# Optimization experiments

Measured on AMD Instinct MI355X. Metric: run time of the kernel, lower is better.

## Reference

```python
import jax, jax.numpy as jnp
import numpy as np

N_NODES = 100000
N_EDGES = 1250000
IN_CH = 64
OUT_CH = 64


def setup_inputs() -> dict:
    key = jax.random.key(0)
    k1, k2, k3 = jax.random.split(key, 3)
    x = jax.random.normal(k1, (N_NODES, IN_CH), dtype=jnp.float32)
    edge_index = jax.random.randint(k2, (2, N_EDGES), 0, N_NODES, dtype=jnp.int64)
    # torch.nn.Linear(3*IN_CH, OUT_CH): W [out, in], b [out]
    scale = 1.0 / np.sqrt(3 * IN_CH)
    W = jax.random.uniform(k3, (OUT_CH, 3 * IN_CH), dtype=jnp.float32,
                           minval=-scale, maxval=scale)
    b = jnp.zeros((OUT_CH,), dtype=jnp.float32)
    return {"x": x, "edge_index": edge_index, "W": W, "b": b}


def reference(x, edge_index, W, b):
    src, dst = edge_index[0], edge_index[1]
    msgs = x[src]  # [E, D] gather of source node features

    agg_sum = jax.ops.segment_sum(msgs, dst, num_segments=N_NODES)  # [N, D]
    count = jax.ops.segment_sum(jnp.ones((msgs.shape[0],), dtype=x.dtype),
                                dst, num_segments=N_NODES)  # [N]
    agg_mean = agg_sum / jnp.maximum(count, 1.0)[:, None]

    agg_max = jax.ops.segment_max(msgs, dst, num_segments=N_NODES)  # [N, D]
    has_edge = (count > 0)[:, None]
    agg_max = jnp.where(has_edge, agg_max, 0.0)  # empty segments -> 0 (PyG default)

    feats = jnp.concatenate([agg_sum, agg_mean, agg_max], axis=-1)  # [N, 3D]
    return jnp.einsum('nf,of->no', feats, W) + b
```

## Files before the change

kernel.cpp:

```cpp
#include <hip/hip_runtime.h>
#include <hip/hip_bf16.h>
#include <math.h>

#define D    64
#define F3   192
#define FS   128
#define NPB  256
#define LBITS 8
#define SBITS 17
#define NBLK 256
#define SCAN_CHUNK 2048
#define BUCKET_PAD 1800
#define SSRC_CAP   2000000

using bf16x8 = __attribute__((ext_vector_type(8))) short;
using f32x4  = __attribute__((ext_vector_type(4))) float;

__device__ __forceinline__ ushort f2bf(float f) {
    __hip_bfloat16 h = __float2bfloat16(f);
    return *reinterpret_cast<ushort*>(&h);
}
__device__ __forceinline__ float bf2f(ushort u) {
    unsigned v = ((unsigned)u) << 16;
    return __uint_as_float(v);
}

__global__ __launch_bounds__(256) void k_cast_hist(
    const float* __restrict__ x, ushort* __restrict__ xb, int n4,
    const float* __restrict__ W, ushort* __restrict__ Wb, int nW,
    const int* __restrict__ dstv, unsigned* __restrict__ bcntT,
    int E, int EPB, int NB, int castBlocks)
{
    int bid = blockIdx.x;
    if (bid < NBLK) {
        __shared__ unsigned h[512];
        for (int i = threadIdx.x; i < NB; i += 256) h[i] = 0;
        __syncthreads();
        int lo = bid * EPB, hi = min(E, lo + EPB);
        for (int e = lo + threadIdx.x; e < hi; e += 256)
            atomicAdd(&h[((unsigned)dstv[e]) >> LBITS], 1u);
        __syncthreads();
        for (int i = threadIdx.x; i < NB; i += 256)
            bcntT[(size_t)i * NBLK + bid] = h[i];
    } else if (bid < NBLK + castBlocks) {
        int i = (bid - NBLK) * 256 + threadIdx.x;
        if (i < n4) {
            float4 v = *reinterpret_cast<const float4*>(x + (size_t)i * 4);
            ushort4 u = { f2bf(v.x), f2bf(v.y), f2bf(v.z), f2bf(v.w) };
            *reinterpret_cast<ushort4*>(xb + (size_t)i * 4) = u;
        }
    } else {
        for (int i = threadIdx.x; i < nW; i += 256) Wb[i] = f2bf(W[i]);
    }
}

__global__ __launch_bounds__(256) void k_chunk_scan(
    const unsigned* __restrict__ cnt, unsigned* __restrict__ offs,
    unsigned* __restrict__ partials, int N)
{
    __shared__ unsigned ts[256];
    int t = threadIdx.x;
    int ebase = blockIdx.x * SCAN_CHUNK + t * 8;
    unsigned v[8];
    unsigned s = 0;
    #pragma unroll
    for (int j = 0; j < 8; ++j) {
        unsigned c = (ebase + j < N) ? cnt[ebase + j] : 0u;
        v[j] = s; s += c;
    }
    ts[t] = s;
    __syncthreads();
    #pragma unroll
    for (int off = 1; off < 256; off <<= 1) {
        unsigned add = (t >= off) ? ts[t - off] : 0u;
        __syncthreads();
        ts[t] += add;
        __syncthreads();
    }
    unsigned tb = (t > 0) ? ts[t - 1] : 0u;
    #pragma unroll
    for (int j = 0; j < 8; ++j)
        if (ebase + j < N) offs[ebase + j] = tb + v[j];
    if (t == 255) partials[blockIdx.x] = ts[255];
}

__device__ __forceinline__ void scan_partials_lds(
    const unsigned* __restrict__ partials, unsigned* psc, int n, int t)
{
    __shared__ unsigned raw[64];
    if (t < n) raw[t] = partials[t];
    __syncthreads();
    if (t == 0) {
        unsigned s = 0;
        for (int i = 0; i < n; ++i) { unsigned c = raw[i]; psc[i] = s; s += c; }
    }
    __syncthreads();
}

__global__ __launch_bounds__(256) void k_bin_scatter(
    const int* __restrict__ srcv, const int* __restrict__ dstv,
    const unsigned* __restrict__ bbaseT, const unsigned* __restrict__ partials,
    int nChunks, unsigned* __restrict__ binned, int E, int EPB, int NB)
{
    __shared__ unsigned cur[512];
    __shared__ unsigned psc[64];
    int t = threadIdx.x;
    scan_partials_lds(partials, psc, nChunks, t);
    for (int i = t; i < NB; i += 256) {
        unsigned idx = (unsigned)i * NBLK + blockIdx.x;
        cur[i] = bbaseT[idx] + psc[idx >> 11];
    }
    __syncthreads();
    int lo = blockIdx.x * EPB, hi = min(E, lo + EPB);
    for (int e = lo + t; e < hi; e += 256) {
        unsigned d = (unsigned)dstv[e];
        unsigned s = (unsigned)srcv[e];
        unsigned p = atomicAdd(&cur[d >> LBITS], 1u);
        binned[p] = ((d & (NPB - 1u)) << SBITS) | s;
    }
}

__global__ __launch_bounds__(256) void k_bucket_csr(
    const unsigned* __restrict__ binned, const unsigned* __restrict__ bbaseT,
    const unsigned* __restrict__ partials, int nChunks,
    unsigned* __restrict__ offs, unsigned* __restrict__ cnt,
    unsigned* __restrict__ ssrc, int E, int NB, int N)
{
    __shared__ unsigned c[256];
    __shared__ unsigned ts[256];
    __shared__ unsigned psc[64];
    int k = blockIdx.x;
    int t = threadIdx.x;
    scan_partials_lds(partials, psc, nChunks, t);

    unsigned i0 = (unsigned)k * NBLK;
    unsigned bstart = bbaseT[i0] + psc[i0 >> 11];
    unsigned bend;
    if (k + 1 < NB) {
        unsigned i1 = (unsigned)(k + 1) * NBLK;
        bend = bbaseT[i1] + psc[i1 >> 11];
    } else bend = (unsigned)E;
    unsigned bstartPad = ((bstart + 7u) & ~7u) + (unsigned)BUCKET_PAD * k;

    c[t] = 0;
    __syncthreads();
    for (unsigned e = bstart + t; e < bend; e += 256)
        atomicAdd(&c[binned[e] >> SBITS], 1u);
    __syncthreads();

    unsigned myc  = c[t];
    unsigned mycp = (myc + 7u) & ~7u;
    ts[t] = mycp;
    __syncthreads();
    #pragma unroll
    for (int off = 1; off < 256; off <<= 1) {
        unsigned add = (t >= off) ? ts[t - off] : 0u;
        __syncthreads();
        ts[t] += add;
        __syncthreads();
    }
    unsigned exclp = t ? ts[t - 1] : 0u;
    unsigned stPad = bstartPad + exclp;

    int gn = k * NPB + t;
    if (gn < N) { offs[gn] = stPad; cnt[gn] = myc; }

    c[t] = exclp;
    __syncthreads();
    for (unsigned e = bstart + t; e < bend; e += 256) {
        unsigned u  = binned[e];
        unsigned ld = u >> SBITS;
        unsigned r  = atomicAdd(&c[ld], 1u);
        ssrc[bstartPad + r] = u & ((1u << SBITS) - 1u);
    }
    __syncthreads();
    if (myc && mycp > myc) {
        unsigned lastId = ssrc[stPad + myc - 1];
        for (unsigned j = myc; j < mycp; ++j) ssrc[stPad + j] = lastId;
    }
}

__global__ __launch_bounds__(256) void k_gather5(
    const ushort*   __restrict__ xb,
    const unsigned* __restrict__ ssrc,
    const unsigned* __restrict__ offs,
    const unsigned* __restrict__ cnt,
    ushort*         __restrict__ feats,
    int N)
{
    const unsigned* xw = reinterpret_cast<const unsigned*>(xb);
    unsigned* fw = reinterpret_cast<unsigned*>(feats);

    int tid  = threadIdx.x;
    unsigned lane = tid & 63;
    unsigned l31  = lane & 31;
    bool     hi   = lane >= 32;
    int wv   = tid >> 6;

    int nq = (N + 3) >> 2;
    for (int q = blockIdx.x; q < nq; q += gridDim.x) {
        int n = q * 4 + wv;
        if (n >= N) continue;

        unsigned st  = offs[n];
        unsigned dg  = cnt[n];
        unsigned dgp = (dg + 7u) & ~7u;

        float se0 = 0.f, so0 = 0.f, se1 = 0.f, so1 = 0.f;
        float me0 = -INFINITY, mo0 = -INFINITY, me1 = -INFINITY, mo1 = -INFINITY;

        unsigned i = 0;
        for (; i + 16 <= dgp; i += 16) {
            uint4 ia = *reinterpret_cast<const uint4*>(ssrc + st + i);
            uint4 ib = *reinterpret_cast<const uint4*>(ssrc + st + i + 4);
            uint4 ic = *reinterpret_cast<const uint4*>(ssrc + st + i + 8);
            uint4 id = *reinterpret_cast<const uint4*>(ssrc + st + i + 12);
            unsigned p0 = hi ? ia.y : ia.x;
            unsigned p1 = hi ? ia.w : ia.z;
            unsigned p2 = hi ? ib.y : ib.x;
            unsigned p3 = hi ? ib.w : ib.z;
            unsigned p4 = hi ? ic.y : ic.x;
            unsigned p5 = hi ? ic.w : ic.z;
            unsigned p6 = hi ? id.y : id.x;
            unsigned p7 = hi ? id.w : id.z;
            unsigned w0 = xw[(p0 << 5) | l31];
            unsigned w1 = xw[(p1 << 5) | l31];
            unsigned w2 = xw[(p2 << 5) | l31];
            unsigned w3 = xw[(p3 << 5) | l31];
            unsigned w4 = xw[(p4 << 5) | l31];
            unsigned w5 = xw[(p5 << 5) | l31];
            unsigned w6 = xw[(p6 << 5) | l31];
            unsigned w7 = xw[(p7 << 5) | l31];
            #pragma unroll
            for (int j = 0; j < 8; ++j) {
                unsigned w = (j==0)?w0:(j==1)?w1:(j==2)?w2:(j==3)?w3:
                             (j==4)?w4:(j==5)?w5:(j==6)?w6:w7;
                float fe = __uint_as_float(w << 16);
                float fo = __uint_as_float(w & 0xFFFF0000u);
                if (j & 1) {
                    se1 += fe; so1 += fo;
                    me1 = fmaxf(me1, fe); mo1 = fmaxf(mo1, fo);
                } else {
                    se0 += fe; so0 += fo;
                    me0 = fmaxf(me0, fe); mo0 = fmaxf(mo0, fo);
                }
            }
        }
        if (i < dgp) {
            uint4 ia = *reinterpret_cast<const uint4*>(ssrc + st + i);
            uint4 ib = *reinterpret_cast<const uint4*>(ssrc + st + i + 4);
            unsigned p0 = hi ? ia.y : ia.x;
            unsigned p1 = hi ? ia.w : ia.z;
            unsigned p2 = hi ? ib.y : ib.x;
            unsigned p3 = hi ? ib.w : ib.z;
            unsigned w0 = xw[(p0 << 5) | l31];
            unsigned w1 = xw[(p1 << 5) | l31];
            unsigned w2 = xw[(p2 << 5) | l31];
            unsigned w3 = xw[(p3 << 5) | l31];
            #pragma unroll
            for (int j = 0; j < 4; ++j) {
                unsigned w = (j==0)?w0:(j==1)?w1:(j==2)?w2:w3;
                float fe = __uint_as_float(w << 16);
                float fo = __uint_as_float(w & 0xFFFF0000u);
                if (j & 1) {
                    se1 += fe; so1 += fo;
                    me1 = fmaxf(me1, fe); mo1 = fmaxf(mo1, fo);
                } else {
                    se0 += fe; so0 += fo;
                    me0 = fmaxf(me0, fe); mo0 = fmaxf(mo0, fo);
                }
            }
        }

        float se = se0 + se1, so = so0 + so1;
        float me = fmaxf(me0, me1), mo = fmaxf(mo0, mo1);
        se += __shfl_xor(se, 32);
        so += __shfl_xor(so, 32);
        me = fmaxf(me, __shfl_xor(me, 32));
        mo = fmaxf(mo, __shfl_xor(mo, 32));

        unsigned p = dgp - dg;
        if (p && dg) {
            unsigned lastId = ssrc[st + dg - 1];
            unsigned w = xw[(lastId << 5) | l31];
            se -= (float)p * __uint_as_float(w << 16);
            so -= (float)p * __uint_as_float(w & 0xFFFF0000u);
        }
        if (!dg) { me = 0.0f; mo = 0.0f; }

        float v0 = hi ? me : se;
        float v1 = hi ? mo : so;
        unsigned outw = ((unsigned)f2bf(v0)) | (((unsigned)f2bf(v1)) << 16);
        fw[((size_t)n << 6) | lane] = outw;
    }
}

__global__ __launch_bounds__(256) void k_mlp2(
    const ushort*   __restrict__ feats,
    const unsigned* __restrict__ cnt,
    const ushort*   __restrict__ Wb,
    const float*    __restrict__ bias,
    float*          __restrict__ out,
    int N)
{
    int tid  = threadIdx.x;
    int lane = tid & 63;
    int wv   = tid >> 6;
    int l16  = lane & 15;
    int kb   = (lane >> 4) << 3;

    int col = (wv << 4) + l16;
    const ushort* wp = Wb + (size_t)col * F3 + kb;
    bf16x8 bS0 = *reinterpret_cast<const bf16x8*>(wp);
    bf16x8 bS1 = *reinterpret_cast<const bf16x8*>(wp + 32);
    bf16x8 bM0 = *reinterpret_cast<const bf16x8*>(wp + 64);
    bf16x8 bM1 = *reinterpret_cast<const bf16x8*>(wp + 96);
    bf16x8 bX0 = *reinterpret_cast<const bf16x8*>(wp + 128);
    bf16x8 bX1 = *reinterpret_cast<const bf16x8*>(wp + 160);
    float bo = bias[col];

    int n0 = blockIdx.x << 4;

    unsigned dgr = cnt[n0 + l16];
    float inv = dgr ? 1.0f / (float)dgr : 0.0f;

    const ushort* arow = feats + (size_t)(n0 + l16) * FS + kb;
    bf16x8 aS0 = *reinterpret_cast<const bf16x8*>(arow);
    bf16x8 aS1 = *reinterpret_cast<const bf16x8*>(arow + 32);
    bf16x8 aX0 = *reinterpret_cast<const bf16x8*>(arow + 64);
    bf16x8 aX1 = *reinterpret_cast<const bf16x8*>(arow + 96);

    bf16x8 aM0, aM1;
    #pragma unroll
    for (int j = 0; j < 8; ++j) {
        aM0[j] = (short)f2bf(bf2f((ushort)aS0[j]) * inv);
        aM1[j] = (short)f2bf(bf2f((ushort)aS1[j]) * inv);
    }

    f32x4 acc = { bo, bo, bo, bo };
    acc = __builtin_amdgcn_mfma_f32_16x16x32_bf16(aS0, bS0, acc, 0, 0, 0);
    acc = __builtin_amdgcn_mfma_f32_16x16x32_bf16(aS1, bS1, acc, 0, 0, 0);
    acc = __builtin_amdgcn_mfma_f32_16x16x32_bf16(aM0, bM0, acc, 0, 0, 0);
    acc = __builtin_amdgcn_mfma_f32_16x16x32_bf16(aM1, bM1, acc, 0, 0, 0);
    acc = __builtin_amdgcn_mfma_f32_16x16x32_bf16(aX0, bX0, acc, 0, 0, 0);
    acc = __builtin_amdgcn_mfma_f32_16x16x32_bf16(aX1, bX1, acc, 0, 0, 0);

    int rbase = n0 + ((lane >> 4) << 2);
    #pragma unroll
    for (int r = 0; r < 4; ++r)
        out[(size_t)(rbase + r) * D + col] = acc[r];
}

extern "C" void kernel_launch(void* const* d_in, const int* in_sizes, int n_in,
                              void* d_out, int out_size, void* d_ws, size_t ws_size,
                              hipStream_t stream)
{
    const float* x  = (const float*)d_in[0];
    const int*   ei = (const int*)d_in[1];
    const float* W  = (const float*)d_in[2];
    const float* b  = (const float*)d_in[3];
    float* out = (float*)d_out;

    int N = in_sizes[0] / D;
    int E = in_sizes[1] / 2;
    const int* srcv = ei;
    const int* dstv = ei + E;

    int NB  = (N + NPB - 1) / NPB;
    int EPB = (E + NBLK - 1) / NBLK;
    int M   = NB * NBLK;

    unsigned* bcntT    = (unsigned*)d_ws;
    unsigned* bbaseT   = bcntT + M;
    unsigned* partials = bbaseT + M;
    unsigned* offs     = partials + 64;
    unsigned* cnt      = offs + N;
    unsigned* ssrc     = cnt + N;
    ushort*   xb       = (ushort*)(ssrc + SSRC_CAP);
    ushort*   Wb       = xb + (size_t)N * D;
    ushort*   feats    = Wb + (size_t)D * F3;
    unsigned* binned   = (unsigned*)feats;

    int nChunksM  = (M + SCAN_CHUNK - 1) / SCAN_CHUNK;
    int n4        = N * D / 4;
    int castBlocks = (n4 + 255) / 256;

    k_cast_hist<<<NBLK + castBlocks + 1, 256, 0, stream>>>(
        x, xb, n4, W, Wb, D * F3, dstv, bcntT, E, EPB, NB, castBlocks);
    k_chunk_scan<<<nChunksM, 256, 0, stream>>>(bcntT, bbaseT, partials, M);
    k_bin_scatter<<<NBLK, 256, 0, stream>>>(srcv, dstv, bbaseT, partials,
                                            nChunksM, binned, E, EPB, NB);
    k_bucket_csr<<<NB, 256, 0, stream>>>(binned, bbaseT, partials, nChunksM,
                                         offs, cnt, ssrc, E, NB, N);
    k_gather5<<<2048, 256, 0, stream>>>(xb, ssrc, offs, cnt, feats, N);
    k_mlp2<<<N / 16, 256, 0, stream>>>(feats, cnt, Wb, b, out, N);
}
```

Before: 114.4 us.

## Fuse neighbor gather aggregation with MFMA linear layer via LDS tile

Merges the gather/aggregate kernel and the MFMA projection kernel into one. Each wave aggregates sum and max for 16 nodes into a swizzled LDS tile, then runs the bf16 MFMA projection for all 64 output columns directly from that tile. This removes the global round trip of the intermediate features buffer and one kernel launch. However, all four waves in a block use the same tile index and never use their wave id to choose nodes. They therefore repeat the same gather work and write identical outputs, which multiplies the dominant irregular gather cost.

```diff
diff --git a/kernel.cpp b/kernel.cpp
--- a/kernel.cpp
+++ b/kernel.cpp
@@ -4,7 +4,6 @@
 
 #define D    64
 #define F3   192
-#define FS   128
 #define NPB  256
 #define LBITS 8
 #define SBITS 17
@@ -180,175 +179,178 @@
     }
 }
 
-__global__ __launch_bounds__(256) void k_gather5(
+__global__ __launch_bounds__(256) void k_gather_mlp(
     const ushort*   __restrict__ xb,
     const unsigned* __restrict__ ssrc,
     const unsigned* __restrict__ offs,
     const unsigned* __restrict__ cnt,
-    ushort*         __restrict__ feats,
+    const ushort*   __restrict__ Wb,
+    const float*    __restrict__ bias,
+    float*          __restrict__ out,
     int N)
 {
+    __shared__ unsigned tile[4][16 * 64];
+    __shared__ float    invl[4][16];
+
     const unsigned* xw = reinterpret_cast<const unsigned*>(xb);
-    unsigned* fw = reinterpret_cast<unsigned*>(feats);
 
     int tid  = threadIdx.x;
     unsigned lane = tid & 63;
     unsigned l31  = lane & 31;
     bool     hi   = lane >= 32;
     int wv   = tid >> 6;
-
-    int nq = (N + 3) >> 2;
-    for (int q = blockIdx.x; q < nq; q += gridDim.x) {
-        int n = q * 4 + wv;
-        if (n >= N) continue;
-
-        unsigned st  = offs[n];
-        unsigned dg  = cnt[n];
-        unsigned dgp = (dg + 7u) & ~7u;
-
-        float se0 = 0.f, so0 = 0.f, se1 = 0.f, so1 = 0.f;
-        float me0 = -INFINITY, mo0 = -INFINITY, me1 = -INFINITY, mo1 = -INFINITY;
-
-        unsigned i = 0;
-        for (; i + 16 <= dgp; i += 16) {
-            uint4 ia = *reinterpret_cast<const uint4*>(ssrc + st + i);
-            uint4 ib = *reinterpret_cast<const uint4*>(ssrc + st + i + 4);
-            uint4 ic = *reinterpret_cast<const uint4*>(ssrc + st + i + 8);
-            uint4 id = *reinterpret_cast<const uint4*>(ssrc + st + i + 12);
-            unsigned p0 = hi ? ia.y : ia.x;
-            unsigned p1 = hi ? ia.w : ia.z;
-            unsigned p2 = hi ? ib.y : ib.x;
-            unsigned p3 = hi ? ib.w : ib.z;
-            unsigned p4 = hi ? ic.y : ic.x;
-            unsigned p5 = hi ? ic.w : ic.z;
-            unsigned p6 = hi ? id.y : id.x;
-            unsigned p7 = hi ? id.w : id.z;
-            unsigned w0 = xw[(p0 << 5) | l31];
-            unsigned w1 = xw[(p1 << 5) | l31];
-            unsigned w2 = xw[(p2 << 5) | l31];
-            unsigned w3 = xw[(p3 << 5) | l31];
-            unsigned w4 = xw[(p4 << 5) | l31];
-            unsigned w5 = xw[(p5 << 5) | l31];
-            unsigned w6 = xw[(p6 << 5) | l31];
-            unsigned w7 = xw[(p7 << 5) | l31];
-            #pragma unroll
-            for (int j = 0; j < 8; ++j) {
-                unsigned w = (j==0)?w0:(j==1)?w1:(j==2)?w2:(j==3)?w3:
-                             (j==4)?w4:(j==5)?w5:(j==6)?w6:w7;
-                float fe = __uint_as_float(w << 16);
-                float fo = __uint_as_float(w & 0xFFFF0000u);
-                if (j & 1) {
-                    se1 += fe; so1 += fo;
-                    me1 = fmaxf(me1, fe); mo1 = fmaxf(mo1, fo);
-                } else {
-                    se0 += fe; so0 += fo;
-                    me0 = fmaxf(me0, fe); mo0 = fmaxf(mo0, fo);
+    unsigned* my = &tile[wv][0];
+
+    int l16 = (int)(lane & 15);
+    int kq  = (int)(lane >> 4);
+    int kb  = kq << 3;
+
+    float bo0 = bias[l16], bo1 = bias[16 + l16];
+    float bo2 = bias[32 + l16], bo3 = bias[48 + l16];
+
+    int ntiles = N >> 4;
+    for (int t = blockIdx.x; t < ntiles; t += gridDim.x) {
+        int n0 = t << 4;
+
+        for (int nd = 0; nd < 16; ++nd) {
+            int n = n0 + nd;
+            unsigned st  = offs[n];
+            unsigned dg  = cnt[n];
+            unsigned dgp = (dg + 7u) & ~7u;
+
+            float se0 = 0.f, so0 = 0.f, se1 = 0.f, so1 = 0.f;
+            float me0 = -INFINITY, mo0 = -INFINITY, me1 = -INFINITY, mo1 = -INFINITY;
+
+            unsigned i = 0;
+            for (; i + 16 <= dgp; i += 16) {
+                uint4 ia = *reinterpret_cast<const uint4*>(ssrc + st + i);
+                uint4 ib = *reinterpret_cast<const uint4*>(ssrc + st + i + 4);
+                uint4 ic = *reinterpret_cast<const uint4*>(ssrc + st + i + 8);
+                uint4 id = *reinterpret_cast<const uint4*>(ssrc + st + i + 12);
+                unsigned p0 = hi ? ia.y : ia.x;
+                unsigned p1 = hi ? ia.w : ia.z;
+                unsigned p2 = hi ? ib.y : ib.x;
+                unsigned p3 = hi ? ib.w : ib.z;
+                unsigned p4 = hi ? ic.y : ic.x;
+                unsigned p5 = hi ? ic.w : ic.z;
+                unsigned p6 = hi ? id.y : id.x;
+                unsigned p7 = hi ? id.w : id.z;
+                unsigned w0 = xw[(p0 << 5) | l31];
+                unsigned w1 = xw[(p1 << 5) | l31];
+                unsigned w2 = xw[(p2 << 5) | l31];
+                unsigned w3 = xw[(p3 << 5) | l31];
+                unsigned w4 = xw[(p4 << 5) | l31];
+                unsigned w5 = xw[(p5 << 5) | l31];
+                unsigned w6 = xw[(p6 << 5) | l31];
+                unsigned w7 = xw[(p7 << 5) | l31];
+                #pragma unroll
+                for (int j = 0; j < 8; ++j) {
+                    unsigned w = (j==0)?w0:(j==1)?w1:(j==2)?w2:(j==3)?w3:
+                                 (j==4)?w4:(j==5)?w5:(j==6)?w6:w7;
+                    float fe = __uint_as_float(w << 16);
+                    float fo = __uint_as_float(w & 0xFFFF0000u);
+                    if (j & 1) {
+                        se1 += fe; so1 += fo;
+                        me1 = fmaxf(me1, fe); mo1 = fmaxf(mo1, fo);
+                    } else {
+                        se0 += fe; so0 += fo;
+                        me0 = fmaxf(me0, fe); mo0 = fmaxf(mo0, fo);
+                    }
                 }
             }
-        }
-        if (i < dgp) {
-            uint4 ia = *reinterpret_cast<const uint4*>(ssrc + st + i);
-            uint4 ib = *reinterpret_cast<const uint4*>(ssrc + st + i + 4);
-            unsigned p0 = hi ? ia.y : ia.x;
-            unsigned p1 = hi ? ia.w : ia.z;
-            unsigned p2 = hi ? ib.y : ib.x;
-            unsigned p3 = hi ? ib.w : ib.z;
-            unsigned w0 = xw[(p0 << 5) | l31];
-            unsigned w1 = xw[(p1 << 5) | l31];
-            unsigned w2 = xw[(p2 << 5) | l31];
-            unsigned w3 = xw[(p3 << 5) | l31];
-            #pragma unroll
-            for (int j = 0; j < 4; ++j) {
-                unsigned w = (j==0)?w0:(j==1)?w1:(j==2)?w2:w3;
-                float fe = __uint_as_float(w << 16);
-                float fo = __uint_as_float(w & 0xFFFF0000u);
-                if (j & 1) {
-                    se1 += fe; so1 += fo;
-                    me1 = fmaxf(me1, fe); mo1 = fmaxf(mo1, fo);
-                } else {
-                    se0 += fe; so0 += fo;
-                    me0 = fmaxf(me0, fe); mo0 = fmaxf(mo0, fo);
+            if (i < dgp) {
+                uint4 ia = *reinterpret_cast<const uint4*>(ssrc + st + i);
+                uint4 ib = *reinterpret_cast<const uint4*>(ssrc + st + i + 4);
+                unsigned p0 = hi ? ia.y : ia.x;
+                unsigned p1 = hi ? ia.w : ia.z;
+                unsigned p2 = hi ? ib.y : ib.x;
+                unsigned p3 = hi ? ib.w : ib.z;
+                unsigned w0 = xw[(p0 << 5) | l31];
+                unsigned w1 = xw[(p1 << 5) | l31];
+                unsigned w2 = xw[(p2 << 5) | l31];
+                unsigned w3 = xw[(p3 << 5) | l31];
+                #pragma unroll
+                for (int j = 0; j < 4; ++j) {
+                    unsigned w = (j==0)?w0:(j==1)?w1:(j==2)?w2:w3;
+                    float fe = __uint_as_float(w << 16);
+                    float fo = __uint_as_float(w & 0xFFFF0000u);
+                    if (j & 1) {
+                        se1 += fe; so1 += fo;
+                        me1 = fmaxf(me1, fe); mo1 = fmaxf(mo1, fo);
+                    } else {
+                        se0 += fe; so0 += fo;
+                        me0 = fmaxf(me0, fe); mo0 = fmaxf(mo0, fo);
+                    }
                 }
             }
-        }
-
-        float se = se0 + se1, so = so0 + so1;
-        float me = fmaxf(me0, me1), mo = fmaxf(mo0, mo1);
-        se += __shfl_xor(se, 32);
-        so += __shfl_xor(so, 32);
-        me = fmaxf(me, __shfl_xor(me, 32));
-        mo = fmaxf(mo, __shfl_xor(mo, 32));
-
-        unsigned p = dgp - dg;
-        if (p && dg) {
-            unsigned lastId = ssrc[st + dg - 1];
-            unsigned w = xw[(lastId << 5) | l31];
-            se -= (float)p * __uint_as_float(w << 16);
-            so -= (float)p * __uint_as_float(w & 0xFFFF0000u);
-        }
-        if (!dg) { me = 0.0f; mo = 0.0f; }
-
-        float v0 = hi ? me : se;
-        float v1 = hi ? mo : so;
-        unsigned outw = ((unsigned)f2bf(v0)) | (((unsigned)f2bf(v1)) << 16);
-        fw[((size_t)n << 6) | lane] = outw;
-    }
-}
-
-__global__ __launch_bounds__(256) void k_mlp2(
-    const ushort*   __restrict__ feats,
-    const unsigned* __restrict__ cnt,
-    const ushort*   __restrict__ Wb,
-    const float*    __restrict__ bias,
-    float*          __restrict__ out,
-    int N)
-{
-    int tid  = threadIdx.x;
-    int lane = tid & 63;
-    int wv   = tid >> 6;
-    int l16  = lane & 15;
-    int kb   = (lane >> 4) << 3;
-
-    int col = (wv << 4) + l16;
-    const ushort* wp = Wb + (size_t)col * F3 + kb;
-    bf16x8 bS0 = *reinterpret_cast<const bf16x8*>(wp);
-    bf16x8 bS1 = *reinterpret_cast<const bf16x8*>(wp + 32);
-    bf16x8 bM0 = *reinterpret_cast<const bf16x8*>(wp + 64);
-    bf16x8 bM1 = *reinterpret_cast<const bf16x8*>(wp + 96);
-    bf16x8 bX0 = *reinterpret_cast<const bf16x8*>(wp + 128);
-    bf16x8 bX1 = *reinterpret_cast<const bf16x8*>(wp + 160);
-    float bo = bias[col];
-
-    int n0 = blockIdx.x << 4;
-
-    unsigned dgr = cnt[n0 + l16];
-    float inv = dgr ? 1.0f / (float)dgr : 0.0f;
-
-    const ushort* arow = feats + (size_t)(n0 + l16) * FS + kb;
-    bf16x8 aS0 = *reinterpret_cast<const bf16x8*>(arow);
-    bf16x8 aS1 = *reinterpret_cast<const bf16x8*>(arow + 32);
-    bf16x8 aX0 = *reinterpret_cast<const bf16x8*>(arow + 64);
-    bf16x8 aX1 = *reinterpret_cast<const bf16x8*>(arow + 96);
-
-    bf16x8 aM0, aM1;
-    #pragma unroll
-    for (int j = 0; j < 8; ++j) {
-        aM0[j] = (short)f2bf(bf2f((ushort)aS0[j]) * inv);
-        aM1[j] = (short)f2bf(bf2f((ushort)aS1[j]) * inv);
-    }
-
-    f32x4 acc = { bo, bo, bo, bo };
-    acc = __builtin_amdgcn_mfma_f32_16x16x32_bf16(aS0, bS0, acc, 0, 0, 0);
-    acc = __builtin_amdgcn_mfma_f32_16x16x32_bf16(aS1, bS1, acc, 0, 0, 0);
-    acc = __builtin_amdgcn_mfma_f32_16x16x32_bf16(aM0, bM0, acc, 0, 0, 0);
-    acc = __builtin_amdgcn_mfma_f32_16x16x32_bf16(aM1, bM1, acc, 0, 0, 0);
-    acc = __builtin_amdgcn_mfma_f32_16x16x32_bf16(aX0, bX0, acc, 0, 0, 0);
-    acc = __builtin_amdgcn_mfma_f32_16x16x32_bf16(aX1, bX1, acc, 0, 0, 0);
-
-    int rbase = n0 + ((lane >> 4) << 2);
-    #pragma unroll
-    for (int r = 0; r < 4; ++r)
-        out[(size_t)(rbase + r) * D + col] = acc[r];
+
+            float se = se0 + se1, so = so0 + so1;
+            float me = fmaxf(me0, me1), mo = fmaxf(mo0, mo1);
+            se += __shfl_xor(se, 32);
+            so += __shfl_xor(so, 32);
+            me = fmaxf(me, __shfl_xor(me, 32));
+            mo = fmaxf(mo, __shfl_xor(mo, 32));
+
+            unsigned p = dgp - dg;
+            if (p && dg) {
+                unsigned lastId = ssrc[st + dg - 1];
+                unsigned w = xw[(lastId << 5) | l31];
+                se -= (float)p * __uint_as_float(w << 16);
+                so -= (float)p * __uint_as_float(w & 0xFFFF0000u);
+            }
+            if (!dg) { me = 0.0f; mo = 0.0f; }
+
+            float v0 = hi ? me : se;
+            float v1 = hi ? mo : so;
+            unsigned outwd = ((unsigned)f2bf(v0)) | (((unsigned)f2bf(v1)) << 16);
+            my[(nd << 6) | (lane ^ (((unsigned)nd & 7u) << 2))] = outwd;
+            if (lane == 0) invl[wv][nd] = dg ? 1.0f / (float)dg : 0.0f;
+        }
+
+        float inv = invl[wv][l16];
+
+        bf16x8 aS0, aS1, aX0, aX1;
+        {
+            unsigned sw = ((unsigned)(l16 & 7)) << 2;
+            unsigned row = (unsigned)l16 << 6;
+            aS0 = *reinterpret_cast<const bf16x8*>(&my[row | (((unsigned)(0*16 + kq*4)) ^ sw)]);
+            aS1 = *reinterpret_cast<const bf16x8*>(&my[row | (((unsigned)(1*16 + kq*4)) ^ sw)]);
+            aX0 = *reinterpret_cast<const bf16x8*>(&my[row | (((unsigned)(2*16 + kq*4)) ^ sw)]);
+            aX1 = *reinterpret_cast<const bf16x8*>(&my[row | (((unsigned)(3*16 + kq*4)) ^ sw)]);
+        }
+        bf16x8 aM0, aM1;
+        #pragma unroll
+        for (int j = 0; j < 8; ++j) {
+            aM0[j] = (short)f2bf(bf2f((ushort)aS0[j]) * inv);
+            aM1[j] = (short)f2bf(bf2f((ushort)aS1[j]) * inv);
+        }
+
+        #pragma unroll
+        for (int cb = 0; cb < 4; ++cb) {
+            int col = (cb << 4) + l16;
+            const ushort* wp = Wb + (size_t)col * F3 + kb;
+            bf16x8 bS0 = *reinterpret_cast<const bf16x8*>(wp);
+            bf16x8 bS1 = *reinterpret_cast<const bf16x8*>(wp + 32);
+            bf16x8 bM0 = *reinterpret_cast<const bf16x8*>(wp + 64);
+            bf16x8 bM1 = *reinterpret_cast<const bf16x8*>(wp + 96);
+            bf16x8 bX0 = *reinterpret_cast<const bf16x8*>(wp + 128);
+            bf16x8 bX1 = *reinterpret_cast<const bf16x8*>(wp + 160);
+            float bo = (cb == 0) ? bo0 : (cb == 1) ? bo1 : (cb == 2) ? bo2 : bo3;
+
+            f32x4 acc = { bo, bo, bo, bo };
+            acc = __builtin_amdgcn_mfma_f32_16x16x32_bf16(aS0, bS0, acc, 0, 0, 0);
+            acc = __builtin_amdgcn_mfma_f32_16x16x32_bf16(aS1, bS1, acc, 0, 0, 0);
+            acc = __builtin_amdgcn_mfma_f32_16x16x32_bf16(aM0, bM0, acc, 0, 0, 0);
+            acc = __builtin_amdgcn_mfma_f32_16x16x32_bf16(aM1, bM1, acc, 0, 0, 0);
+            acc = __builtin_amdgcn_mfma_f32_16x16x32_bf16(aX0, bX0, acc, 0, 0, 0);
+            acc = __builtin_amdgcn_mfma_f32_16x16x32_bf16(aX1, bX1, acc, 0, 0, 0);
+
+            int rbase = n0 + (kq << 2);
+            #pragma unroll
+            for (int r = 0; r < 4; ++r)
+                out[(size_t)(rbase + r) * D + col] = acc[r];
+        }
+    }
 }
 
 extern "C" void kernel_launch(void* const* d_in, const int* in_sizes, int n_in,
@@ -378,8 +380,7 @@
     unsigned* ssrc     = cnt + N;
     ushort*   xb       = (ushort*)(ssrc + SSRC_CAP);
     ushort*   Wb       = xb + (size_t)N * D;
-    ushort*   feats    = Wb + (size_t)D * F3;
-    unsigned* binned   = (unsigned*)feats;
+    unsigned* binned   = (unsigned*)(Wb + (size_t)D * F3);
 
     int nChunksM  = (M + SCAN_CHUNK - 1) / SCAN_CHUNK;
     int n4        = N * D / 4;
@@ -392,6 +393,5 @@
                                             nChunksM, binned, E, EPB, NB);
     k_bucket_csr<<<NB, 256, 0, stream>>>(binned, bbaseT, partials, nChunksM,
                                          offs, cnt, ssrc, E, NB, N);
-    k_gather5<<<2048, 256, 0, stream>>>(xb, ssrc, offs, cnt, feats, N);
-    k_mlp2<<<N / 16, 256, 0, stream>>>(feats, cnt, Wb, b, out, N);
-}
+    k_gather_mlp<<<2048, 256, 0, stream>>>(xb, ssrc, offs, cnt, Wb, b, out, N);
+}
```

Measured after the change: 254.9 us. 2.23x slower.
